# Kernel optimization log

Hardware: AMD Instinct MI355X
Metric: run time of the kernel (lower is better)

Reference implementation:

```python
import jax, jax.numpy as jnp
import numpy as np

NB, T, N, C = 8, 8, 6890, 128
CLASS_NUM = 7
D_SUM = 512
PCADIM = 64
V = 7702  # garment template vertex count
EPS = 1e-5


def setup_inputs() -> dict:
    key = jax.random.key(0)
    ks = jax.random.split(key, 12)
    f = lambda k, s: jax.random.normal(k, s, dtype=jnp.float32)
    return {
        "x": f(ks[0], (NB, T, N, 3)),
        "sem_logits": f(ks[1], (NB * T, N, CLASS_NUM)),
        "feature": f(ks[2], (NB * T, C, N)),
        "garment_summary": f(ks[3], (NB, T, D_SUM)),
        "W1": f(ks[4], (128, D_SUM)) * 0.02, "b1": jnp.zeros((128,), jnp.float32),
        "g1": jnp.ones((128,), jnp.float32), "be1": jnp.zeros((128,), jnp.float32),
        "rm1": jnp.zeros((128,), jnp.float32), "rv1": jnp.ones((128,), jnp.float32),
        "W2": f(ks[5], (64, 128)) * 0.02, "b2": jnp.zeros((64,), jnp.float32),
        "g2": jnp.ones((64,), jnp.float32), "be2": jnp.zeros((64,), jnp.float32),
        "rm2": jnp.zeros((64,), jnp.float32), "rv2": jnp.ones((64,), jnp.float32),
        "W3": f(ks[6], (PCADIM, 64)) * 0.02, "b3": jnp.zeros((PCADIM,), jnp.float32),
        "pca_comp": f(ks[7], (PCADIM, V * 3)) * 0.02,
        "pca_mean": f(ks[8], (V * 3,)) * 0.02,
        "pca_scale": jnp.abs(f(ks[9], (V * 3,))) + 0.5,
        "garment_label": 1,
        "n": N // 4,
    }


def _segmentation_gather(x, sem_logits, feature, garment_label, n):
    # Vectorized form of the per-sample boolean-mask select / truncate / zero-pad loop.
    # x: [B,N,3]; feature: [B,C,N]; sem_logits: [B,N,K]
    feat = jnp.swapaxes(feature, 1, 2)                     # [B,N,C]
    labels = jnp.argmax(sem_logits, axis=2)                # [B,N] (detached in original)
    mask = labels == garment_label                         # [B,N]
    count = mask.sum(axis=1)                               # [B]
    # stable argsort puts selected (mask=True -> key False=0) indices first, in order
    order = jnp.argsort(jnp.logical_not(mask), axis=1)[:, :n]   # [B,n]
    valid = (jnp.arange(n)[None, :] < count[:, None]).astype(x.dtype)  # [B,n]
    gv = jnp.take_along_axis(x, order[:, :, None], axis=1) * valid[:, :, None]
    gf = jnp.take_along_axis(feat, order[:, :, None], axis=1) * valid[:, :, None]
    return gv, gf


def reference(x, sem_logits, feature, garment_summary, W1, b1, g1, be1, rm1, rv1,
              W2, b2, g2, be2, rm2, rv2, W3, b3, pca_comp, pca_mean, pca_scale,
              garment_label, n):
    nbatch, t = x.shape[0], x.shape[1]
    xf = x.reshape(nbatch * t, -1, 3)
    garment_v, garment_f = _segmentation_gather(xf, sem_logits, feature, garment_label, n)

    # PCAEncoder: 1x1 Conv1d over a length-1 sequence == linear layers; BN in eval mode
    def bn(h, g, be, rm, rv):
        return (h - rm) * jax.lax.rsqrt(rv + EPS) * g + be

    gs = garment_summary.max(axis=1)                       # [nbatch, 512] (max over T)
    h = jax.nn.relu(bn(gs @ W1.T + b1, g1, be1, rm1, rv1))
    h = jax.nn.relu(bn(h @ W2.T + b2, g2, be2, rm2, rv2))
    coeff = h @ W3.T + b3                                  # [nbatch, PCADIM]

    # PCA_inverse_transform
    tpose = ((coeff @ pca_comp) + pca_mean) * pca_scale
    tpose = tpose.reshape(coeff.shape[0], -1, 3)           # [nbatch, V, 3]
    return garment_v, garment_f, coeff, tpose
```

## Files before the change

kernel.cpp:

```cpp
#include <hip/hip_runtime.h>

#define NBATCH   8
#define TT       8
#define NPTS     6890
#define KCLS     7
#define CCH      128
#define BSAMP    64
#define NOUT     1722
#define DSUM     512
#define PCADIM   64
#define V3       23106
#define EPSBN    1e-5f

#define NW       108
#define PCH      128
#define NCHK     54
#define CHB      2
#define CHN      64
#define LDSQ     129
#define CPG      6
#define NGRP     9
#define K4B      91
#define NGATHER  (BSAMP * CHB * NGRP)

#define OFF_GV     0
#define OFF_GF     (BSAMP * NOUT * 3)
#define OFF_COEFF  (OFF_GF + BSAMP * NOUT * CCH)
#define OFF_TPOSE  (OFF_COEFF + NBATCH * PCADIM)

__global__ __launch_bounds__(256) void k_prep(
    const float* __restrict__ logits,
    const int*   __restrict__ d_label,
    const float* __restrict__ x,
    unsigned long long* __restrict__ ws_mask,
    float* __restrict__ gv,
    int*   __restrict__ ws_spref,
    int*   __restrict__ ws_count,
    const float* __restrict__ gsum,
    const float* __restrict__ W1, const float* __restrict__ b1,
    const float* __restrict__ g1, const float* __restrict__ be1,
    const float* __restrict__ rm1, const float* __restrict__ rv1,
    const float* __restrict__ W2, const float* __restrict__ b2,
    const float* __restrict__ g2, const float* __restrict__ be2,
    const float* __restrict__ rm2, const float* __restrict__ rv2,
    const float* __restrict__ W3, const float* __restrict__ b3,
    float* __restrict__ coeff_out, float* __restrict__ coeff_ws)
{
    const int tid = threadIdx.x;

    if (blockIdx.x < BSAMP) {
        const int b = blockIdx.x;
        const int label = d_label[0];
        __shared__ unsigned long long smask[NW];
        __shared__ int spref[NW + 1];

        const float* lb = logits + (size_t)b * NPTS * KCLS;
        #pragma unroll 1
        for (int r = 0; r < 27; ++r) {
            const int i = r * 256 + tid;
            bool sel = false;
            if (i < NPTS) {
                const float* p = lb + (size_t)i * KCLS;
                float best = p[0]; int bi = 0;
                #pragma unroll
                for (int k = 1; k < KCLS; ++k) {
                    float v = p[k];
                    if (v > best) { best = v; bi = k; }
                }
                sel = (bi == label);
            }
            const unsigned long long m = __ballot(sel);
            if ((tid & 63) == 0) {
                const int w = r * 4 + (tid >> 6);
                if (w < NW) smask[w] = m;
            }
        }
        __syncthreads();

        if (tid == 0) {
            int run = 0;
            for (int w = 0; w < NW; ++w) { spref[w] = run; run += __popcll(smask[w]); }
            spref[NW] = run;
            ws_count[b] = run < NOUT ? run : NOUT;
        }
        __syncthreads();
        if (tid < NW) {
            ws_mask [b * NW + tid] = smask[tid];
            ws_spref[b * NW + tid] = spref[tid];
        }

        const float* xb = x + (size_t)b * NPTS * 3;
        for (int i = tid; i < NPTS; i += 256) {
            const int w = i >> 6, lb6 = i & 63;
            const unsigned long long m = smask[w];
            if ((m >> lb6) & 1ull) {
                const int pos = spref[w] + __popcll(m & ((1ull << lb6) - 1ull));
                if (pos < NOUT) {
                    const size_t go = ((size_t)b * NOUT + pos) * 3;
                    gv[go + 0] = xb[(size_t)i * 3 + 0];
                    gv[go + 1] = xb[(size_t)i * 3 + 1];
                    gv[go + 2] = xb[(size_t)i * 3 + 2];
                }
            }
        }

        int cnt = spref[NW]; if (cnt > NOUT) cnt = NOUT;
        for (int j = cnt + tid; j < NOUT; j += 256) {
            float* gp = gv + ((size_t)b * NOUT + j) * 3;
            gp[0] = 0.f; gp[1] = 0.f; gp[2] = 0.f;
        }
    } else {
        const int s    = blockIdx.x - BSAMP;
        const int lane = tid & 63;
        const int wv   = tid >> 6;

        __shared__ float gs[DSUM];
        __shared__ float h1[128];
        __shared__ float h2[64];

        for (int d = tid; d < DSUM; d += 256) {
            const float* p = gsum + ((size_t)s * TT) * DSUM + d;
            float m = p[0];
            #pragma unroll
            for (int t = 1; t < TT; ++t) m = fmaxf(m, p[(size_t)t * DSUM]);
            gs[d] = m;
        }
        __syncthreads();

        for (int r = 0; r < 32; r += 2) {
            const int j0 = wv * 32 + r, j1 = j0 + 1;
            const float* w0 = W1 + (size_t)j0 * DSUM;
            const float* w1 = W1 + (size_t)j1 * DSUM;
            float pa = 0.f, pb = 0.f;
            #pragma unroll
            for (int d = lane; d < DSUM; d += 64) {
                const float gd = gs[d];
                pa = fmaf(w0[d], gd, pa);
                pb = fmaf(w1[d], gd, pb);
            }
            #pragma unroll
            for (int off = 32; off; off >>= 1) {
                pa += __shfl_xor(pa, off);
                pb += __shfl_xor(pb, off);
            }
            if (lane == 0) {
                pa += b1[j0];
                pa = (pa - rm1[j0]) * rsqrtf(rv1[j0] + EPSBN) * g1[j0] + be1[j0];
                h1[j0] = fmaxf(pa, 0.f);
                pb += b1[j1];
                pb = (pb - rm1[j1]) * rsqrtf(rv1[j1] + EPSBN) * g1[j1] + be1[j1];
                h1[j1] = fmaxf(pb, 0.f);
            }
        }
        __syncthreads();

        for (int r = 0; r < 16; ++r) {
            const int jj = wv * 16 + r;
            const float* w = W2 + (size_t)jj * 128;
            float p = w[lane] * h1[lane] + w[lane + 64] * h1[lane + 64];
            #pragma unroll
            for (int off = 32; off; off >>= 1) p += __shfl_xor(p, off);
            if (lane == 0) {
                p += b2[jj];
                p = (p - rm2[jj]) * rsqrtf(rv2[jj] + EPSBN) * g2[jj] + be2[jj];
                h2[jj] = fmaxf(p, 0.f);
            }
        }
        __syncthreads();

        for (int r = 0; r < 16; ++r) {
            const int jj = wv * 16 + r;
            float p = W3[(size_t)jj * 64 + lane] * h2[lane];
            #pragma unroll
            for (int off = 32; off; off >>= 1) p += __shfl_xor(p, off);
            if (lane == 0) {
                p += b3[jj];
                coeff_out[s * PCADIM + jj] = p;
                coeff_ws[s * PCADIM + jj]  = p;
            }
        }
    }
}

__global__ __launch_bounds__(256, 4) void k_gather(
    const float* __restrict__ feature,
    const unsigned long long* __restrict__ ws_mask,
    const int* __restrict__ ws_spref,
    const int* __restrict__ ws_count,
    float* __restrict__ gf,
    const float* __restrict__ coeff_ws,
    const float* __restrict__ comp,
    const float* __restrict__ mean_,
    const float* __restrict__ scale_,
    float* __restrict__ tpose)
{
    __shared__ float lds[CHN * LDSQ];
    __shared__ int   spos[PCH];
    __shared__ int   sel_list[PCH];
    __shared__ int   s_ns[2];

    const int tid = threadIdx.x;

    if (blockIdx.x < K4B) {
        float* sc = lds;
        for (int o = tid; o < NBATCH * PCADIM; o += 256) sc[o] = coeff_ws[o];
        __syncthreads();

        const int v = blockIdx.x * 256 + tid;
        if (v >= V3) return;

        float acc[NBATCH];
        #pragma unroll
        for (int s = 0; s < NBATCH; ++s) acc[s] = 0.f;
        for (int k = 0; k < PCADIM; ++k) {
            const float pv = comp[(size_t)k * V3 + v];
            #pragma unroll
            for (int s = 0; s < NBATCH; ++s)
                acc[s] = fmaf(sc[s * PCADIM + k], pv, acc[s]);
        }
        const float mn = mean_[v], scl = scale_[v];
        #pragma unroll
        for (int s = 0; s < NBATCH; ++s)
            tpose[(size_t)s * V3 + v] = (acc[s] + mn) * scl;
        return;
    }

    const int gb  = blockIdx.x - K4B;
    const int b   = gb / (CHB * NGRP);
    const int rem = gb % (CHB * NGRP);
    const int cb  = rem / NGRP;
    const int g   = rem % NGRP;

    const int lane = tid & 63;
    const int cg   = tid >> 6;
    const int p0   = lane * 2;
    const float* fbase = feature + ((size_t)b * CCH + cb * CHN) * NPTS;

    float2 rc[16], rn[16];

    {
        const int i0 = g * (CPG * PCH);
        const int il = min(PCH, NPTS - i0);
        const float* fb = fbase + i0 + p0;
        if (p0 < il) {
            #pragma unroll
            for (int it = 0; it < 16; ++it)
                rc[it] = *(const float2*)(fb + (size_t)(cg * 16 + it) * NPTS);
        } else {
            #pragma unroll
            for (int it = 0; it < 16; ++it) rc[it] = make_float2(0.f, 0.f);
        }
    }

    {
        const int cnt  = ws_count[b];
        const int tail = NOUT - cnt;
        if (tail > 0) {
            const int nshares = CHB * NGRP;
            const int share = (tail + nshares - 1) / nshares;
            const int idx   = cb * NGRP + g;
            const int r0    = cnt + idx * share;
            const int r1    = min(r0 + share, NOUT);
            const int nrows = r1 - r0;
            if (nrows > 0) {
                float4* base4 = (float4*)(gf + ((size_t)b * NOUT + r0) * CCH);
                const int total = nrows * 32;
                for (int f = tid; f < total; f += 256)
                    base4[f] = make_float4(0.f, 0.f, 0.f, 0.f);
            }
        }
    }

    #pragma unroll
    for (int c = 0; c < CPG; ++c) {
        const int chunk = g * CPG + c;

        if (c + 1 < CPG) {
            const int i1 = (chunk + 1) * PCH;
            const int il = min(PCH, NPTS - i1);
            const float* fb = fbase + i1 + p0;
            if (p0 < il) {
                #pragma unroll
                for (int it = 0; it < 16; ++it)
                    rn[it] = *(const float2*)(fb + (size_t)(cg * 16 + it) * NPTS);
            } else {
                #pragma unroll
                for (int it = 0; it < 16; ++it) rn[it] = make_float2(0.f, 0.f);
            }
        }

        __syncthreads();

        #pragma unroll
        for (int it = 0; it < 16; ++it) {
            const int cch = cg * 16 + it;
            lds[cch * LDSQ + p0]     = rc[it].x;
            lds[cch * LDSQ + p0 + 1] = rc[it].y;
        }

        if (tid < 128) {
            const int w    = tid >> 6;
            const int word = 2 * chunk + w;
            const unsigned long long m = ws_mask[b * NW + word];
            const int base = ws_spref[b * NW + word];
            const int sel  = (int)((m >> lane) & 1ull);
            const int pos  = base + __popcll(m & ((1ull << lane) - 1ull));
            const int sp   = (sel && pos < NOUT) ? pos : -1;
            spos[tid] = sp;
            const unsigned long long mm = __ballot(sp >= 0);
            const int before = __popcll(mm & ((1ull << lane) - 1ull));
            if (sp >= 0) sel_list[w * 64 + before] = tid;
            if (lane == 0) s_ns[w] = __popcll(mm);
        }
        __syncthreads();

        const int rw = tid >> 6;
        #pragma unroll 1
        for (int w = 0; w < 2; ++w) {
            const int ns = s_ns[w];
            for (int s = rw; s < ns; s += 4) {
                const int p   = sel_list[w * 64 + s];
                const int pos = spos[p];
                gf[((size_t)b * NOUT + pos) * CCH + cb * CHN + lane] =
                    lds[lane * LDSQ + p];
            }
        }

        if (c + 1 < CPG) {
            #pragma unroll
            for (int it = 0; it < 16; ++it) rc[it] = rn[it];
        }
    }
}

extern "C" void kernel_launch(void* const* d_in, const int* in_sizes, int n_in,
                              void* d_out, int out_size, void* d_ws, size_t ws_size,
                              hipStream_t stream) {
    const float* x      = (const float*)d_in[0];
    const float* logits = (const float*)d_in[1];
    const float* feat   = (const float*)d_in[2];
    const float* gsum   = (const float*)d_in[3];
    const float* W1  = (const float*)d_in[4];
    const float* b1  = (const float*)d_in[5];
    const float* g1  = (const float*)d_in[6];
    const float* be1 = (const float*)d_in[7];
    const float* rm1 = (const float*)d_in[8];
    const float* rv1 = (const float*)d_in[9];
    const float* W2  = (const float*)d_in[10];
    const float* b2  = (const float*)d_in[11];
    const float* g2  = (const float*)d_in[12];
    const float* be2 = (const float*)d_in[13];
    const float* rm2 = (const float*)d_in[14];
    const float* rv2 = (const float*)d_in[15];
    const float* W3  = (const float*)d_in[16];
    const float* b3  = (const float*)d_in[17];
    const float* comp  = (const float*)d_in[18];
    const float* mean_ = (const float*)d_in[19];
    const float* scale_= (const float*)d_in[20];
    const int* d_label = (const int*)d_in[21];

    float* out   = (float*)d_out;
    float* gv    = out + OFF_GV;
    float* gf    = out + OFF_GF;
    float* coeff = out + OFF_COEFF;
    float* tpose = out + OFF_TPOSE;

    unsigned long long* ws_mask = (unsigned long long*)d_ws;
    int*   ws_spref = (int*)(ws_mask + BSAMP * NW);
    int*   ws_count = ws_spref + BSAMP * NW;
    float* coeff_ws = (float*)(ws_count + BSAMP);

    k_prep  <<<BSAMP + NBATCH,  256, 0, stream>>>(logits, d_label, x, ws_mask, gv,
                                                  ws_spref, ws_count,
                                                  gsum, W1, b1, g1, be1, rm1, rv1,
                                                  W2, b2, g2, be2, rm2, rv2, W3, b3,
                                                  coeff, coeff_ws);
    k_gather<<<K4B + NGATHER,   256, 0, stream>>>(feat, ws_mask, ws_spref, ws_count,
                                                  gf, coeff_ws, comp, mean_, scale_,
                                                  tpose);
}
```

Before: 92.03 us.

## Parallelize mask argmax across many blocks and move prefix scan into gather kernel

Measured after the change: 93.84 us. No clear change (+2.0%).

```diff
diff --git a/kernel.cpp b/kernel.cpp
--- a/kernel.cpp
+++ b/kernel.cpp
@@ -14,13 +14,13 @@
 
 #define NW       108
 #define PCH      128
-#define NCHK     54
 #define CHB      2
 #define CHN      64
 #define LDSQ     129
-#define CPG      6
-#define NGRP     9
+#define CPG      9
+#define NGRP     6
 #define K4B      91
+#define NSCAN    BSAMP
 #define NGATHER  (BSAMP * CHB * NGRP)
 
 #define OFF_GV     0
@@ -28,14 +28,10 @@
 #define OFF_COEFF  (OFF_GF + BSAMP * NOUT * CCH)
 #define OFF_TPOSE  (OFF_COEFF + NBATCH * PCADIM)
 
-__global__ __launch_bounds__(256) void k_prep(
+__global__ __launch_bounds__(256) void k1_mask_mlp(
     const float* __restrict__ logits,
     const int*   __restrict__ d_label,
-    const float* __restrict__ x,
     unsigned long long* __restrict__ ws_mask,
-    float* __restrict__ gv,
-    int*   __restrict__ ws_spref,
-    int*   __restrict__ ws_count,
     const float* __restrict__ gsum,
     const float* __restrict__ W1, const float* __restrict__ b1,
     const float* __restrict__ g1, const float* __restrict__ be1,
@@ -48,69 +44,30 @@
 {
     const int tid = threadIdx.x;
 
-    if (blockIdx.x < BSAMP) {
-        const int b = blockIdx.x;
+    if (blockIdx.x < BSAMP * 27) {
+        const int b     = blockIdx.x / 27;
+        const int chunk = blockIdx.x % 27;
+        const int i     = chunk * 256 + tid;
         const int label = d_label[0];
-        __shared__ unsigned long long smask[NW];
-        __shared__ int spref[NW + 1];
-
-        const float* lb = logits + (size_t)b * NPTS * KCLS;
-        #pragma unroll 1
-        for (int r = 0; r < 27; ++r) {
-            const int i = r * 256 + tid;
-            bool sel = false;
-            if (i < NPTS) {
-                const float* p = lb + (size_t)i * KCLS;
-                float best = p[0]; int bi = 0;
-                #pragma unroll
-                for (int k = 1; k < KCLS; ++k) {
-                    float v = p[k];
-                    if (v > best) { best = v; bi = k; }
-                }
-                sel = (bi == label);
-            }
-            const unsigned long long m = __ballot(sel);
-            if ((tid & 63) == 0) {
-                const int w = r * 4 + (tid >> 6);
-                if (w < NW) smask[w] = m;
-            }
-        }
-        __syncthreads();
-
-        if (tid == 0) {
-            int run = 0;
-            for (int w = 0; w < NW; ++w) { spref[w] = run; run += __popcll(smask[w]); }
-            spref[NW] = run;
-            ws_count[b] = run < NOUT ? run : NOUT;
-        }
-        __syncthreads();
-        if (tid < NW) {
-            ws_mask [b * NW + tid] = smask[tid];
-            ws_spref[b * NW + tid] = spref[tid];
-        }
-
-        const float* xb = x + (size_t)b * NPTS * 3;
-        for (int i = tid; i < NPTS; i += 256) {
-            const int w = i >> 6, lb6 = i & 63;
-            const unsigned long long m = smask[w];
-            if ((m >> lb6) & 1ull) {
-                const int pos = spref[w] + __popcll(m & ((1ull << lb6) - 1ull));
-                if (pos < NOUT) {
-                    const size_t go = ((size_t)b * NOUT + pos) * 3;
-                    gv[go + 0] = xb[(size_t)i * 3 + 0];
-                    gv[go + 1] = xb[(size_t)i * 3 + 1];
-                    gv[go + 2] = xb[(size_t)i * 3 + 2];
-                }
-            }
-        }
-
-        int cnt = spref[NW]; if (cnt > NOUT) cnt = NOUT;
-        for (int j = cnt + tid; j < NOUT; j += 256) {
-            float* gp = gv + ((size_t)b * NOUT + j) * 3;
-            gp[0] = 0.f; gp[1] = 0.f; gp[2] = 0.f;
+
+        bool sel = false;
+        if (i < NPTS) {
+            const float* p = logits + ((size_t)b * NPTS + i) * KCLS;
+            float best = p[0]; int bi = 0;
+            #pragma unroll
+            for (int k = 1; k < KCLS; ++k) {
+                float v = p[k];
+                if (v > best) { best = v; bi = k; }
+            }
+            sel = (bi == label);
+        }
+        const unsigned long long m = __ballot(sel);
+        if ((tid & 63) == 0) {
+            const int w = chunk * 4 + (tid >> 6);
+            if (w < NW) ws_mask[b * NW + w] = m;
         }
     } else {
-        const int s    = blockIdx.x - BSAMP;
+        const int s    = blockIdx.x - BSAMP * 27;
         const int lane = tid & 63;
         const int wv   = tid >> 6;
 
@@ -182,11 +139,11 @@
     }
 }
 
-__global__ __launch_bounds__(256, 4) void k_gather(
+__global__ __launch_bounds__(256, 4) void k2_all(
     const float* __restrict__ feature,
     const unsigned long long* __restrict__ ws_mask,
-    const int* __restrict__ ws_spref,
-    const int* __restrict__ ws_count,
+    const float* __restrict__ x,
+    float* __restrict__ gv,
     float* __restrict__ gf,
     const float* __restrict__ coeff_ws,
     const float* __restrict__ comp,
@@ -195,9 +152,12 @@
     float* __restrict__ tpose)
 {
     __shared__ float lds[CHN * LDSQ];
-    __shared__ int   spos[PCH];
-    __shared__ int   sel_list[PCH];
-    __shared__ int   s_ns[2];
+    __shared__ unsigned long long smask[NW];
+    __shared__ int  swc[NW];
+    __shared__ int  spos[PCH];
+    __shared__ int  sel_list[PCH];
+    __shared__ int  s_ns[2];
+    __shared__ int  s_cnt;
 
     const int tid = threadIdx.x;
 
@@ -225,7 +185,42 @@
         return;
     }
 
-    const int gb  = blockIdx.x - K4B;
+    if (blockIdx.x < K4B + NSCAN) {
+        const int b = blockIdx.x - K4B;
+
+        if (tid < NW) smask[tid] = ws_mask[b * NW + tid];
+        __syncthreads();
+        if (tid < NW) swc[tid] = __popcll(smask[tid]);
+        __syncthreads();
+        if (tid == 0) {
+            int run = 0;
+            for (int w = 0; w < NW; ++w) { int t = swc[w]; swc[w] = run; run += t; }
+            s_cnt = run < NOUT ? run : NOUT;
+        }
+        __syncthreads();
+
+        const float* xb = x + (size_t)b * NPTS * 3;
+        for (int i = tid; i < NPTS; i += 256) {
+            const int w = i >> 6, lb6 = i & 63;
+            const unsigned long long m = smask[w];
+            if ((m >> lb6) & 1ull) {
+                const int pos = swc[w] + __popcll(m & ((1ull << lb6) - 1ull));
+                if (pos < NOUT) {
+                    const size_t go = ((size_t)b * NOUT + pos) * 3;
+                    gv[go + 0] = xb[(size_t)i * 3 + 0];
+                    gv[go + 1] = xb[(size_t)i * 3 + 1];
+                    gv[go + 2] = xb[(size_t)i * 3 + 2];
+                }
+            }
+        }
+        for (int j = s_cnt + tid; j < NOUT; j += 256) {
+            float* gp = gv + ((size_t)b * NOUT + j) * 3;
+            gp[0] = 0.f; gp[1] = 0.f; gp[2] = 0.f;
+        }
+        return;
+    }
+
+    const int gb  = blockIdx.x - (K4B + NSCAN);
     const int b   = gb / (CHB * NGRP);
     const int rem = gb % (CHB * NGRP);
     const int cb  = rem / NGRP;
@@ -252,8 +247,19 @@
         }
     }
 
+    if (tid < NW) smask[tid] = ws_mask[b * NW + tid];
+    __syncthreads();
+    if (tid < NW) swc[tid] = __popcll(smask[tid]);
+    __syncthreads();
+    if (tid == 0) {
+        int run = 0;
+        for (int w = 0; w < NW; ++w) { int t = swc[w]; swc[w] = run; run += t; }
+        s_cnt = run < NOUT ? run : NOUT;
+    }
+    __syncthreads();
+
     {
-        const int cnt  = ws_count[b];
+        const int cnt  = s_cnt;
         const int tail = NOUT - cnt;
         if (tail > 0) {
             const int nshares = CHB * NGRP;
@@ -271,7 +277,7 @@
         }
     }
 
-    #pragma unroll
+    #pragma unroll 1
     for (int c = 0; c < CPG; ++c) {
         const int chunk = g * CPG + c;
 
@@ -301,8 +307,8 @@
         if (tid < 128) {
             const int w    = tid >> 6;
             const int word = 2 * chunk + w;
-            const unsigned long long m = ws_mask[b * NW + word];
-            const int base = ws_spref[b * NW + word];
+            const unsigned long long m = smask[word];
+            const int base = swc[word];
             const int sel  = (int)((m >> lane) & 1ull);
             const int pos  = base + __popcll(m & ((1ull << lane) - 1ull));
             const int sp   = (sel && pos < NOUT) ? pos : -1;
@@ -366,16 +372,12 @@
     float* tpose = out + OFF_TPOSE;
 
     unsigned long long* ws_mask = (unsigned long long*)d_ws;
-    int*   ws_spref = (int*)(ws_mask + BSAMP * NW);
-    int*   ws_count = ws_spref + BSAMP * NW;
-    float* coeff_ws = (float*)(ws_count + BSAMP);
-
-    k_prep  <<<BSAMP + NBATCH,  256, 0, stream>>>(logits, d_label, x, ws_mask, gv,
-                                                  ws_spref, ws_count,
-                                                  gsum, W1, b1, g1, be1, rm1, rv1,
-                                                  W2, b2, g2, be2, rm2, rv2, W3, b3,
-                                                  coeff, coeff_ws);
-    k_gather<<<K4B + NGATHER,   256, 0, stream>>>(feat, ws_mask, ws_spref, ws_count,
-                                                  gf, coeff_ws, comp, mean_, scale_,
-                                                  tpose);
+    float* coeff_ws = (float*)(ws_mask + BSAMP * NW);
+
+    k1_mask_mlp<<<BSAMP * 27 + NBATCH, 256, 0, stream>>>(
+        logits, d_label, ws_mask, gsum, W1, b1, g1, be1, rm1, rv1,
+        W2, b2, g2, be2, rm2, rv2, W3, b3, coeff, coeff_ws);
+
+    k2_all<<<K4B + NSCAN + NGATHER, 256, 0, stream>>>(
+        feat, ws_mask, x, gv, gf, coeff_ws, comp, mean_, scale_, tpose);
 }
```
